# Optimization experiments

Measured on AMD Instinct MI355X. Metric: run time of the kernel, lower is better.

Reference implementation:

```python
import jax, jax.numpy as jnp
import numpy as np

N = 8192
F_IN = 256
F_OUT = 256
EDGE_P = 0.002  # avg degree ~16 before self-loops


def setup_inputs() -> dict:
    key = jax.random.key(0)
    k_a, k_x, k_w, k_b = jax.random.split(key, 4)
    # symmetric 0/1 dense adjacency, no self loops (added in reference as I + A)
    u = jax.random.uniform(k_a, (N, N))
    A = (u < EDGE_P).astype(jnp.float32)
    A = jnp.maximum(A, A.T)
    A = A * (1.0 - jnp.eye(N, dtype=jnp.float32))
    inputs = jax.random.normal(k_x, (N, F_IN), dtype=jnp.float32)
    # matches torch init: rand/100 - 0.005 in [-0.005, 0.005)
    weight = jax.random.uniform(k_w, (F_IN, F_OUT), dtype=jnp.float32) / 100.0 - 0.005
    bias = jax.random.uniform(k_b, (F_OUT,), dtype=jnp.float32) / 100.0 - 0.005
    return {"A": A, "inputs": inputs, "weight": weight, "bias": bias}


def reference(A, inputs, weight, bias):
    # A_ = I + A
    A_ = A + jnp.eye(A.shape[0], dtype=A.dtype)
    # D^{-1/2}: the original builds diag matrices and does dense GEMMs;
    # row/col scaling is the same math, expressed efficiently.
    d = jnp.sum(A_, axis=1) ** (-0.5)  # [N]
    norm_A = d[:, None] * A_ * d[None, :]  # D^{-1/2} (I+A) D^{-1/2}
    out = norm_A @ inputs @ weight + bias  # [N, F_OUT]
    return out  # activation is None
```

## Files before the change

kernel.cpp:

```cpp
#include <hip/hip_runtime.h>
#include <hip/hip_bf16.h>
#include <cstdint>


#define NN 8192
#define FF 256
#define ELLK 128
#define BM 64
#define BN 64
#define BK 16
#define NGEMM ((NN / BM) * (FF / BN))
#define NSCAN (NN / 2)

__device__ __forceinline__ float bf2f(unsigned short u) {
    union { unsigned int i; float f; } c; c.i = ((unsigned int)u) << 16; return c.f;
}
__device__ __forceinline__ unsigned short f2bf(float f) {
    union { float f; unsigned int i; } c; c.f = f;
    unsigned int r = c.i + 0x7FFF + ((c.i >> 16) & 1);
    return (unsigned short)(r >> 16);
}

__device__ __forceinline__ void scan_row_upper(const float* __restrict__ A, int r,
                                               unsigned short* __restrict__ loc,
                                               int* __restrict__ lcnt) {
    const uint4* Arow = reinterpret_cast<const uint4*>(A + (size_t)r * NN);
    const int c0 = (r + 1) >> 2;
    for (int c = c0 + threadIdx.x; c < NN / 4; c += 256) {
        uint4 v = Arow[c];
        if (v.x | v.y | v.z | v.w) {
            int base = c * 4;
            if (v.x && base + 0 > r) { int p = atomicAdd(lcnt, 1); if (p < ELLK) loc[p] = (unsigned short)(base + 0); }
            if (v.y && base + 1 > r) { int p = atomicAdd(lcnt, 1); if (p < ELLK) loc[p] = (unsigned short)(base + 1); }
            if (v.z && base + 2 > r) { int p = atomicAdd(lcnt, 1); if (p < ELLK) loc[p] = (unsigned short)(base + 2); }
            if (v.w && base + 3 > r) { int p = atomicAdd(lcnt, 1); if (p < ELLK) loc[p] = (unsigned short)(base + 3); }
        }
    }
}

__global__ __launch_bounds__(256) void fused_stage1(const float* __restrict__ A,
                                                    const float* __restrict__ X,
                                                    const float* __restrict__ W,
                                                    unsigned short* __restrict__ Yb,
                                                    int* __restrict__ cnt,
                                                    unsigned short* __restrict__ ell) {
    if (blockIdx.x < NGEMM) {
        __shared__ float As[BK][BM + 4];
        __shared__ float Bs[BK][BN];
        const int bid = blockIdx.x;
        const int m0 = (bid / (FF / BN)) * BM;
        const int n0 = (bid % (FF / BN)) * BN;
        const int tid = threadIdx.x;
        const int tr = tid / 16;
        const int tc = tid % 16;
        float acc[4][4] = {};
        for (int k0 = 0; k0 < FF; k0 += BK) {
            {
                int r  = tid / 4;
                int kq = (tid % 4) * 4;
                float4 v = *reinterpret_cast<const float4*>(X + (size_t)(m0 + r) * FF + k0 + kq);
                As[kq + 0][r] = v.x; As[kq + 1][r] = v.y; As[kq + 2][r] = v.z; As[kq + 3][r] = v.w;
            }
            {
                int kk = tid / 16;
                int nq = (tid % 16) * 4;
                float4 v = *reinterpret_cast<const float4*>(W + (size_t)(k0 + kk) * FF + n0 + nq);
                *reinterpret_cast<float4*>(&Bs[kk][nq]) = v;
            }
            __syncthreads();
            #pragma unroll
            for (int kk = 0; kk < BK; ++kk) {
                float a[4], b[4];
                #pragma unroll
                for (int i = 0; i < 4; ++i) a[i] = As[kk][tr * 4 + i];
                #pragma unroll
                for (int j = 0; j < 4; ++j) b[j] = Bs[kk][tc * 4 + j];
                #pragma unroll
                for (int i = 0; i < 4; ++i)
                    #pragma unroll
                    for (int j = 0; j < 4; ++j)
                        acc[i][j] = fmaf(a[i], b[j], acc[i][j]);
            }
            __syncthreads();
        }
        #pragma unroll
        for (int i = 0; i < 4; ++i) {
            ushort4 v = { f2bf(acc[i][0]), f2bf(acc[i][1]), f2bf(acc[i][2]), f2bf(acc[i][3]) };
            *reinterpret_cast<ushort4*>(Yb + (size_t)(m0 + tr * 4 + i) * FF + n0 + tc * 4) = v;
        }
    } else {
        __shared__ unsigned short loc0[ELLK], loc1[ELLK];
        __shared__ int lc0, lc1, base0, base1;
        const int s  = blockIdx.x - NGEMM;
        const int r0 = s;
        const int r1 = NN - 1 - s;
        if (threadIdx.x == 0) { lc0 = 0; lc1 = 0; }
        __syncthreads();
        scan_row_upper(A, r0, loc0, &lc0);
        scan_row_upper(A, r1, loc1, &lc1);
        __syncthreads();
        const int n0 = lc0 < ELLK ? lc0 : ELLK;
        const int n1 = lc1 < ELLK ? lc1 : ELLK;
        if (threadIdx.x == 0) base0 = atomicAdd(&cnt[r0], n0);
        if (threadIdx.x == 1) base1 = atomicAdd(&cnt[r1], n1);
        __syncthreads();
        for (int t = threadIdx.x; t < n0; t += 256) {
            int p = base0 + t;
            if (p < ELLK) ell[(size_t)r0 * ELLK + p] = loc0[t];
        }
        for (int t = threadIdx.x; t < n1; t += 256) {
            int p = base1 + t;
            if (p < ELLK) ell[(size_t)r1 * ELLK + p] = loc1[t];
        }
        for (int t = threadIdx.x; t < n0; t += 256) {
            int j = loc0[t];
            int q = atomicAdd(&cnt[j], 1);
            if (q < ELLK) ell[(size_t)j * ELLK + q] = (unsigned short)r0;
        }
        for (int t = threadIdx.x; t < n1; t += 256) {
            int j = loc1[t];
            int q = atomicAdd(&cnt[j], 1);
            if (q < ELLK) ell[(size_t)j * ELLK + q] = (unsigned short)r1;
        }
    }
}

__global__ __launch_bounds__(256) void spmm_kernel(const unsigned short* __restrict__ Yb,
                                                   const int* __restrict__ cnt,
                                                   const unsigned short* __restrict__ ell,
                                                   const float* __restrict__ bias,
                                                   float* __restrict__ out) {
    const int wave = threadIdx.x >> 6;
    const int lane = threadIdx.x & 63;
    const int row = blockIdx.x * 4 + wave;
    __shared__ unsigned short sidx[4][ELLK];
    __shared__ float sdj[4][ELLK];
    int c = cnt[row];
    c = c < ELLK ? c : ELLK;
    for (int t = lane; t < c; t += 64) {
        int j = ell[(size_t)row * ELLK + t];
        sidx[wave][t] = (unsigned short)j;
        sdj[wave][t]  = rsqrtf((float)(cnt[j] + 1));
    }
    __syncthreads();
    const float di = rsqrtf((float)(c + 1));
    ushort4 ys = *reinterpret_cast<const ushort4*>(Yb + (size_t)row * FF + lane * 4);
    float a0 = di * bf2f(ys.x), a1 = di * bf2f(ys.y);
    float a2 = di * bf2f(ys.z), a3 = di * bf2f(ys.w);
    for (int t = 0; t < c; ++t) {
        int j = sidx[wave][t];
        float dj = sdj[wave][t];
        ushort4 v = *reinterpret_cast<const ushort4*>(Yb + (size_t)j * FF + lane * 4);
        a0 = fmaf(dj, bf2f(v.x), a0);
        a1 = fmaf(dj, bf2f(v.y), a1);
        a2 = fmaf(dj, bf2f(v.z), a2);
        a3 = fmaf(dj, bf2f(v.w), a3);
    }
    float4 b4 = *reinterpret_cast<const float4*>(bias + lane * 4);
    float4 o;
    o.x = fmaf(di, a0, b4.x);
    o.y = fmaf(di, a1, b4.y);
    o.z = fmaf(di, a2, b4.z);
    o.w = fmaf(di, a3, b4.w);
    *reinterpret_cast<float4*>(out + (size_t)row * FF + lane * 4) = o;
}

extern "C" void kernel_launch(void* const* d_in, const int* in_sizes, int n_in,
                              void* d_out, int out_size, void* d_ws, size_t ws_size,
                              hipStream_t stream) {
    const float* A    = (const float*)d_in[0];
    const float* X    = (const float*)d_in[1];
    const float* W    = (const float*)d_in[2];
    const float* bias = (const float*)d_in[3];
    float* out = (float*)d_out;

    char* ws = (char*)d_ws;
    unsigned short* Yb  = (unsigned short*)(ws);
    int*            cnt = (int*)(ws + (size_t)NN * FF * 2);
    unsigned short* ell = (unsigned short*)(ws + (size_t)NN * FF * 2 + NN * 4);

    hipMemsetAsync(cnt, 0, NN * sizeof(int), stream);

    fused_stage1<<<NGEMM + NSCAN, 256, 0, stream>>>(A, X, W, Yb, cnt, ell);
    spmm_kernel<<<NN / 4, 256, 0, stream>>>(Yb, cnt, ell, bias, out);
}
```

Measured before the change: 56.32 us.

## Compute X@W tile with bf16 MFMA instead of scalar FP32 FMAs

Replaces the scalar FP32 register-blocked GEMM in the fused stage-1 kernel with bf16 MFMA 16x16x32 instructions. X and W are converted to bf16 when staged into shared memory, with W stored transposed, and the K loop now steps in 64-wide chunks. This targets the compute cost of the dense GEMM, which runs alongside the adjacency scan blocks. In exchange it rounds the inputs to bf16 before multiplying, which adds precision loss, and the transposed W stores may cause LDS bank conflicts.

```diff
diff --git a/kernel.cpp b/kernel.cpp
--- a/kernel.cpp
+++ b/kernel.cpp
@@ -8,9 +8,11 @@
 #define ELLK 128
 #define BM 64
 #define BN 64
-#define BK 16
 #define NGEMM ((NN / BM) * (FF / BN))
 #define NSCAN (NN / 2)
+
+typedef short bf16x8 __attribute__((ext_vector_type(8)));
+typedef float f32x4  __attribute__((ext_vector_type(4)));
 
 __device__ __forceinline__ float bf2f(unsigned short u) {
     union { unsigned int i; float f; } c; c.i = ((unsigned int)u) << 16; return c.f;
@@ -45,48 +47,67 @@
                                                     int* __restrict__ cnt,
                                                     unsigned short* __restrict__ ell) {
     if (blockIdx.x < NGEMM) {
-        __shared__ float As[BK][BM + 4];
-        __shared__ float Bs[BK][BN];
+        __shared__ unsigned short Xs[64][68];
+        __shared__ unsigned short Wt[64][68];
         const int bid = blockIdx.x;
         const int m0 = (bid / (FF / BN)) * BM;
         const int n0 = (bid % (FF / BN)) * BN;
-        const int tid = threadIdx.x;
-        const int tr = tid / 16;
-        const int tc = tid % 16;
-        float acc[4][4] = {};
-        for (int k0 = 0; k0 < FF; k0 += BK) {
+        const int t  = threadIdx.x;
+        const int w  = t >> 6;
+        const int l  = t & 63;
+        const int lm = l & 15;
+        const int lk = (l >> 4) << 2;
+        f32x4 acc[4] = {};
+        for (int kp = 0; kp < 4; ++kp) {
+            const int kbase = kp * 64;
+            __syncthreads();
             {
-                int r  = tid / 4;
-                int kq = (tid % 4) * 4;
-                float4 v = *reinterpret_cast<const float4*>(X + (size_t)(m0 + r) * FF + k0 + kq);
-                As[kq + 0][r] = v.x; As[kq + 1][r] = v.y; As[kq + 2][r] = v.z; As[kq + 3][r] = v.w;
+                int row = t >> 2;
+                #pragma unroll
+                for (int q = 0; q < 4; ++q) {
+                    int kq = (t & 3) * 4 + q * 16;
+                    float4 v = *reinterpret_cast<const float4*>(X + (size_t)(m0 + row) * FF + kbase + kq);
+                    ushort4 b = { f2bf(v.x), f2bf(v.y), f2bf(v.z), f2bf(v.w) };
+                    *reinterpret_cast<ushort4*>(&Xs[row][kq]) = b;
+                }
             }
             {
-                int kk = tid / 16;
-                int nq = (tid % 16) * 4;
-                float4 v = *reinterpret_cast<const float4*>(W + (size_t)(k0 + kk) * FF + n0 + nq);
-                *reinterpret_cast<float4*>(&Bs[kk][nq]) = v;
+                int n4 = (t & 15) * 4;
+                int kk = t >> 4;
+                #pragma unroll
+                for (int q = 0; q < 4; ++q) {
+                    int k = kk + q * 16;
+                    float4 v = *reinterpret_cast<const float4*>(W + (size_t)(kbase + k) * FF + n0 + n4);
+                    Wt[n4 + 0][k] = f2bf(v.x);
+                    Wt[n4 + 1][k] = f2bf(v.y);
+                    Wt[n4 + 2][k] = f2bf(v.z);
+                    Wt[n4 + 3][k] = f2bf(v.w);
+                }
             }
             __syncthreads();
             #pragma unroll
-            for (int kk = 0; kk < BK; ++kk) {
-                float a[4], b[4];
+            for (int ks = 0; ks < 2; ++ks) {
+                const int k0 = ks * 32;
+                union { bf16x8 v; uint2 u[2]; } af;
+                af.u[0] = *reinterpret_cast<const uint2*>(&Xs[w * 16 + lm][k0 + lk]);
+                af.u[1] = *reinterpret_cast<const uint2*>(&Xs[w * 16 + lm][k0 + 16 + lk]);
                 #pragma unroll
-                for (int i = 0; i < 4; ++i) a[i] = As[kk][tr * 4 + i];
-                #pragma unroll
-                for (int j = 0; j < 4; ++j) b[j] = Bs[kk][tc * 4 + j];
-                #pragma unroll
-                for (int i = 0; i < 4; ++i)
-                    #pragma unroll
-                    for (int j = 0; j < 4; ++j)
-                        acc[i][j] = fmaf(a[i], b[j], acc[i][j]);
-            }
-            __syncthreads();
+                for (int f = 0; f < 4; ++f) {
+                    union { bf16x8 v; uint2 u[2]; } bf;
+                    bf.u[0] = *reinterpret_cast<const uint2*>(&Wt[f * 16 + lm][k0 + lk]);
+                    bf.u[1] = *reinterpret_cast<const uint2*>(&Wt[f * 16 + lm][k0 + 16 + lk]);
+                    acc[f] = __builtin_amdgcn_mfma_f32_16x16x32_bf16(af.v, bf.v, acc[f], 0, 0, 0);
+                }
+            }
         }
         #pragma unroll
-        for (int i = 0; i < 4; ++i) {
-            ushort4 v = { f2bf(acc[i][0]), f2bf(acc[i][1]), f2bf(acc[i][2]), f2bf(acc[i][3]) };
-            *reinterpret_cast<ushort4*>(Yb + (size_t)(m0 + tr * 4 + i) * FF + n0 + tc * 4) = v;
+        for (int f = 0; f < 4; ++f) {
+            #pragma unroll
+            for (int r = 0; r < 4; ++r) {
+                int row = m0 + w * 16 + lk + r;
+                int col = n0 + f * 16 + lm;
+                Yb[(size_t)row * FF + col] = f2bf(acc[f][r]);
+            }
         }
     } else {
         __shared__ unsigned short loc0[ELLK], loc1[ELLK];
```

Measured after the change: 55.01 us. -2.3%, faster.
